# Kernel tuning notes

Measured on AMD Instinct MI355X. Metric: run time of the kernel, lower is better.

The kernel has to match this reference:

```python
import jax, jax.numpy as jnp
import numpy as np

HIDDEN = 1024
INTER = 4096
NUM_EXPERTS = 8
TOP_K = 2


def setup_inputs() -> dict:
    key = jax.random.key(0)
    ks = jax.random.split(key, 6)
    B, S = 4, 2048
    hidden_states = jax.random.normal(ks[0], (B, S, HIDDEN), dtype=jnp.float32)
    scale = 0.02
    # nn.Linear stores weight as [out, in]; y = x @ W.T + b
    gate_w = jax.random.normal(ks[1], (NUM_EXPERTS, HIDDEN), dtype=jnp.float32) * scale
    W1 = jax.random.normal(ks[2], (NUM_EXPERTS, INTER, HIDDEN), dtype=jnp.float32) * scale
    b1 = jax.random.normal(ks[3], (NUM_EXPERTS, INTER), dtype=jnp.float32) * scale
    W2 = jax.random.normal(ks[4], (NUM_EXPERTS, HIDDEN, INTER), dtype=jnp.float32) * scale
    b2 = jax.random.normal(ks[5], (NUM_EXPERTS, HIDDEN), dtype=jnp.float32) * scale
    return {"hidden_states": hidden_states, "gate_w": gate_w,
            "W1": W1, "b1": b1, "W2": W2, "b2": b2}


def reference(hidden_states, gate_w, W1, b1, W2, b2):
    B, S, H = hidden_states.shape
    x = hidden_states.reshape(-1, H)                      # [T, H]
    # Gating: top-k logits -> softmax over the k selected experts only
    gate_logits = x @ gate_w.T                            # [T, E]
    top_vals, top_idx = jax.lax.top_k(gate_logits, TOP_K) # [T, K]
    weights = jax.nn.softmax(top_vals, axis=-1)           # [T, K]
    # Per-token combine weight for each expert (0 if not selected)
    one_hot = jax.nn.one_hot(top_idx, NUM_EXPERTS, dtype=x.dtype)  # [T, K, E]
    combine = jnp.einsum("tk,tke->te", weights, one_hot)           # [T, E]
    # Expert MLPs: fixed small loop over experts (structurally distinct params)
    out = jnp.zeros_like(x)
    for e in range(NUM_EXPERTS):
        h = jax.nn.gelu(x @ W1[e].T + b1[e], approximate=False)  # [T, INTER]
        y = h @ W2[e].T + b2[e]                                   # [T, H]
        out = out + combine[:, e:e + 1] * y
    return out.reshape(B, S, H)
```

## Files before the change

### kernel.cpp

```cpp
#include <hip/hip_runtime.h>
#include <hip/hip_bf16.h>
#include <stdint.h>

#define HID 1024
#define INTER_ 4096
#define NE 8
#define NTOK 8192
#define NPAIR (NTOK * 2)
#define MAXT 72

using f32x4 = __attribute__((ext_vector_type(4))) float;
using bf16x8 = __attribute__((ext_vector_type(8))) __bf16;
using ushort8v = __attribute__((ext_vector_type(8))) unsigned short;

__device__ __forceinline__ unsigned short f2b(float f) {
  unsigned int u = __float_as_uint(f);
  u += 0x7fffu + ((u >> 16) & 1u);
  return (unsigned short)(u >> 16);
}
__device__ __forceinline__ float b2f(unsigned short u) {
  return __uint_as_float((unsigned int)u << 16);
}

__device__ __forceinline__ float gelu_f(float v) {
  float z = fabsf(v) * 0.70710678118654752f;
  float t = __builtin_amdgcn_rcpf(1.f + 0.3275911f * z);
  float p = t * (0.254829592f +
            t * (-0.284496736f +
            t * (1.421413741f +
            t * (-1.453152027f + t * 1.061405429f))));
  float er = 1.f - p * __expf(-z * z);
  er = copysignf(er, v);
  return 0.5f * v * (1.f + er);
}

#define GLD_LDS(gp, lp)                                                        \
  __builtin_amdgcn_global_load_lds(                                            \
      (const __attribute__((address_space(1))) unsigned int*)(const void*)(gp),\
      (__attribute__((address_space(3))) unsigned int*)(void*)(lp), 16, 0, 0)

#define WAITV(N) asm volatile("s_waitcnt vmcnt(" #N ")" ::: "memory")

__global__ __launch_bounds__(256) void gate_kernel(
    const float* __restrict__ x, const float* __restrict__ gw,
    int* __restrict__ topi, float* __restrict__ topw,
    unsigned short* __restrict__ xb)
{
  int gwave = (blockIdx.x * 256 + threadIdx.x) >> 6;
  int lane = threadIdx.x & 63;
  if (gwave >= NTOK) return;
  const float* xr = x + (size_t)gwave * HID;
  unsigned short* xo = xb + (size_t)gwave * HID;
  float acc[NE];
#pragma unroll
  for (int e = 0; e < NE; ++e) acc[e] = 0.f;
#pragma unroll
  for (int q = 0; q < 4; ++q) {
    float4 v = *reinterpret_cast<const float4*>(xr + q * 256 + lane * 4);
    ushort4 uv;
    uv.x = f2b(v.x); uv.y = f2b(v.y); uv.z = f2b(v.z); uv.w = f2b(v.w);
    *reinterpret_cast<ushort4*>(xo + q * 256 + lane * 4) = uv;
#pragma unroll
    for (int e = 0; e < NE; ++e) {
      float4 wv = *reinterpret_cast<const float4*>(gw + e * HID + q * 256 + lane * 4);
      acc[e] += v.x * wv.x + v.y * wv.y + v.z * wv.z + v.w * wv.w;
    }
  }
#pragma unroll
  for (int e = 0; e < NE; ++e) {
#pragma unroll
    for (int off = 32; off > 0; off >>= 1) acc[e] += __shfl_xor(acc[e], off);
  }
  if (lane == 0) {
    float v0 = -1e30f; int i0 = 0;
#pragma unroll
    for (int e = 0; e < NE; ++e) if (acc[e] > v0) { v0 = acc[e]; i0 = e; }
    float v1 = -1e30f; int i1 = 0;
#pragma unroll
    for (int e = 0; e < NE; ++e) if (e != i0 && acc[e] > v1) { v1 = acc[e]; i1 = e; }
    float e1 = __expf(v1 - v0);
    float s = 1.f + e1;
    topi[gwave * 2] = i0; topi[gwave * 2 + 1] = i1;
    topw[gwave * 2] = 1.f / s; topw[gwave * 2 + 1] = e1 / s;
  }
}

__global__ __launch_bounds__(256) void hist_kernel(const int* __restrict__ topi,
                                                   int* __restrict__ bcnt)
{
  int tid = threadIdx.x, blk = blockIdx.x;
  int t = blk * 256 + tid;
  int e0 = topi[t * 2], e1 = topi[t * 2 + 1];
  int w = tid >> 6, lane = tid & 63;
  __shared__ int wcnt[4][NE];
#pragma unroll
  for (int e = 0; e < NE; ++e) {
    unsigned long long m0 = __ballot(e0 == e);
    unsigned long long m1 = __ballot(e1 == e);
    if (lane == 0) wcnt[w][e] = __popcll(m0) + __popcll(m1);
  }
  __syncthreads();
  if (tid < NE) {
    int s = 0;
#pragma unroll
    for (int w2 = 0; w2 < 4; ++w2) s += wcnt[w2][tid];
    bcnt[blk * NE + tid] = s;
  }
}

__global__ void scan2_kernel(const int* __restrict__ bcnt, int* __restrict__ offs,
                             int* __restrict__ tile_e, int* __restrict__ tile_m,
                             int* __restrict__ ntile, int* __restrict__ gbase)
{
  __shared__ int cnts[NE];
  __shared__ int soffs[NE];
  int tid = threadIdx.x;
  if (tid < NE) {
    int s = 0;
#pragma unroll
    for (int b = 0; b < 32; ++b) s += bcnt[b * NE + tid];
    cnts[tid] = s;
  }
  __syncthreads();
  if (tid == 0) {
    int o = 0, tt = 0;
    for (int e = 0; e < NE; ++e) {
      offs[e] = o; soffs[e] = o;
      int c = cnts[e];
      for (int m = 0; m < c; m += 256) { tile_e[tt] = e; tile_m[tt] = m; ++tt; }
      o += c;
    }
    offs[NE] = o;
    *ntile = tt;
  }
  __syncthreads();
  if (tid < 32 * NE) {
    int b = tid >> 3, e = tid & 7;
    int g = soffs[e];
    for (int b2 = 0; b2 < b; ++b2) g += bcnt[b2 * NE + e];
    gbase[b * NE + e] = g;
  }
}

__global__ __launch_bounds__(256) void scatter2_kernel(
    const int* __restrict__ topi, const float* __restrict__ topw,
    const int* __restrict__ gbase,
    int* __restrict__ toklist, float* __restrict__ wlist, int* __restrict__ pos)
{
  int tid = threadIdx.x, blk = blockIdx.x;
  int t = blk * 256 + tid;
  int e0 = topi[t * 2], e1 = topi[t * 2 + 1];
  float w0 = topw[t * 2], w1 = topw[t * 2 + 1];
  int w = tid >> 6, lane = tid & 63;
  unsigned long long lt = (1ull << lane) - 1ull;
  unsigned long long le = lt | (1ull << lane);
  __shared__ int wcnt[4][NE];
  __shared__ int wbase[4][NE];
  int r0 = 0, r1 = 0;
#pragma unroll
  for (int e = 0; e < NE; ++e) {
    unsigned long long m0 = __ballot(e0 == e);
    unsigned long long m1 = __ballot(e1 == e);
    if (lane == 0) wcnt[w][e] = __popcll(m0) + __popcll(m1);
    if (e0 == e) r0 = __popcll(m0 & lt) + __popcll(m1 & lt);
    if (e1 == e) r1 = __popcll(m0 & le) + __popcll(m1 & lt);
  }
  __syncthreads();
  if (tid < 4 * NE) {
    int w2 = tid >> 3, e = tid & 7;
    int b = gbase[blk * NE + e];
    for (int w3 = 0; w3 < w2; ++w3) b += wcnt[w3][e];
    wbase[w2][e] = b;
  }
  __syncthreads();
  int P0 = wbase[w][e0] + r0;
  int P1 = wbase[w][e1] + r1;
  toklist[P0] = t; wlist[P0] = w0; pos[t * 2] = P0;
  toklist[P1] = t; wlist[P1] = w1; pos[t * 2 + 1] = P1;
}

__global__ __launch_bounds__(256) void cvtw_kernel(
    const float* __restrict__ W1, const float* __restrict__ W2,
    unsigned short* __restrict__ w1b, unsigned short* __restrict__ w2b, int n8)
{
  int half = gridDim.x >> 1;
  const float* src = (blockIdx.x < half) ? W1 : W2;
  unsigned short* dst = (blockIdx.x < half) ? w1b : w2b;
  int b0 = (blockIdx.x < half) ? blockIdx.x : blockIdx.x - half;
  int stride = half * 256;
  for (int i = b0 * 256 + threadIdx.x; i < n8; i += stride) {
    const float4* s = reinterpret_cast<const float4*>(src) + (size_t)i * 2;
    float4 a = s[0], b = s[1];
    ushort8v u;
    u[0] = f2b(a.x); u[1] = f2b(a.y); u[2] = f2b(a.z); u[3] = f2b(a.w);
    u[4] = f2b(b.x); u[5] = f2b(b.y); u[6] = f2b(b.z); u[7] = f2b(b.w);
    reinterpret_cast<ushort8v*>(dst)[i] = u;
  }
}


__global__ __launch_bounds__(512, 4) void gemm1_kernel(
    const unsigned short* __restrict__ xb, const unsigned short* __restrict__ w1b,
    const float* __restrict__ b1,
    const int* __restrict__ toklist, const int* __restrict__ offs,
    const int* __restrict__ tile_e, const int* __restrict__ tile_m,
    const int* __restrict__ ntile,
    unsigned short* __restrict__ hb)
{
  const int t = blockIdx.y;
  if (t >= *ntile) return;
  const int e = tile_e[t];
  const int m0 = tile_m[t];
  const int base = offs[e];
  const int cnt = offs[e + 1] - base;
  const int n0 = blockIdx.x * 128;

  __shared__ __align__(16) unsigned short As[3][256 * 32];
  __shared__ __align__(16) unsigned short Bs[3][128 * 32];

  const int tid = threadIdx.x;
  const int lane = tid & 63;
  const int w = tid >> 6;
  const int wr = w >> 1, wc = w & 1;

  const int r0 = tid >> 2;
  const int sl = tid & 3;
  const int scg = sl ^ ((r0 >> 1) & 3);
  const unsigned short* gA[2];
  const unsigned short* gB;
#pragma unroll
  for (int g = 0; g < 2; ++g) {
    int row = g * 128 + r0;
    int mrow = m0 + row; if (mrow >= cnt) mrow = cnt - 1;
    int tk = toklist[base + mrow];
    gA[g] = xb + (size_t)tk * HID + scg * 8;
  }
  gB = w1b + ((size_t)e * INTER_ + n0 + r0) * HID + scg * 8;

  int raq[4], rbq[4];
#pragma unroll
  for (int i = 0; i < 4; ++i) {
    int rA = wr * 64 + i * 16 + (lane & 15);
    raq[i] = rA * 32 + (((lane >> 4) ^ ((rA >> 1) & 3)) * 8);
    int rB = wc * 64 + i * 16 + (lane & 15);
    rbq[i] = rB * 32 + (((lane >> 4) ^ ((rB >> 1) & 3)) * 8);
  }

  f32x4 acc[4][4];
#pragma unroll
  for (int i = 0; i < 4; ++i)
#pragma unroll
    for (int j = 0; j < 4; ++j) acc[i][j] = (f32x4){0.f, 0.f, 0.f, 0.f};

  bf16x8 afr[4], bfr[4];

  auto stage = [&](int slot, int s) {
    const int kof = s * 32;
    GLD_LDS(gA[0] + kof, &As[slot][tid * 8]);
    GLD_LDS(gA[1] + kof, &As[slot][4096 + tid * 8]);
    GLD_LDS(gB + kof,    &Bs[slot][tid * 8]);
  };
  auto load_frags = [&](int slot) {
    const unsigned short* Ab = &As[slot][0];
    const unsigned short* Bb = &Bs[slot][0];
#pragma unroll
    for (int j = 0; j < 4; ++j) bfr[j] = *reinterpret_cast<const bf16x8*>(Bb + rbq[j]);
#pragma unroll
    for (int i = 0; i < 4; ++i) afr[i] = *reinterpret_cast<const bf16x8*>(Ab + raq[i]);
  };
  auto mfma_step = [&]() {
#pragma unroll
    for (int i = 0; i < 4; ++i)
#pragma unroll
      for (int j = 0; j < 4; ++j)
        acc[i][j] = __builtin_amdgcn_mfma_f32_16x16x32_bf16(afr[i], bfr[j], acc[i][j], 0, 0, 0);
  };

  const int NS = HID / 32;
  stage(0, 0); stage(1, 1);
  WAITV(3);
  __builtin_amdgcn_s_barrier();
  load_frags(0);
#pragma unroll 3
  for (int s = 0; s < NS - 2; ++s) {
    stage((s + 2) % 3, s + 2);
    WAITV(3);
    __builtin_amdgcn_s_barrier();
    mfma_step();
    load_frags((s + 1) % 3);
  }
  WAITV(0);
  __builtin_amdgcn_s_barrier();
  mfma_step();
  load_frags((NS - 1) % 3);
  mfma_step();

  float bias[4];
  const int colb = n0 + wc * 64 + (lane & 15);
#pragma unroll
  for (int j = 0; j < 4; ++j) bias[j] = b1[(size_t)e * INTER_ + colb + j * 16];
#pragma unroll
  for (int i = 0; i < 4; ++i) {
    int mbase = m0 + wr * 64 + i * 16 + (lane >> 4) * 4;
#pragma unroll
    for (int r = 0; r < 4; ++r) {
      int m = mbase + r;
      if (m < cnt) {
        unsigned short* hrow = hb + (size_t)(base + m) * INTER_ + colb;
#pragma unroll
        for (int j = 0; j < 4; ++j)
          hrow[j * 16] = f2b(gelu_f(acc[i][j][r] + bias[j]));
      }
    }
  }
}

__global__ __launch_bounds__(512, 4) void gemm2_kernel(
    const unsigned short* __restrict__ hb, const unsigned short* __restrict__ w2b,
    const int* __restrict__ offs,
    const int* __restrict__ tile_e, const int* __restrict__ tile_m,
    const int* __restrict__ ntile,
    unsigned short* __restrict__ part)
{
  const int h = blockIdx.x;
  const int xcd = h & 7;
  const int j = h >> 3;
  const int t = 9 * xcd + j % 9;
  const int nb = j / 9;
  if (t >= *ntile) return;
  const int e = tile_e[t];
  const int m0 = tile_m[t];
  const int base = offs[e];
  const int cnt = offs[e + 1] - base;
  const int n0 = nb * 128;
  const int kbase = blockIdx.z * (INTER_ / 2);

  __shared__ __align__(16) unsigned short As[3][256 * 32];
  __shared__ __align__(16) unsigned short Bs[3][128 * 32];

  const int tid = threadIdx.x;
  const int lane = tid & 63;
  const int w = tid >> 6;
  const int wr = w >> 1, wc = w & 1;

  const int r0 = tid >> 2;
  const int sl = tid & 3;
  const int scg = sl ^ ((r0 >> 1) & 3);
  const unsigned short* gA[2];
  const unsigned short* gB;
#pragma unroll
  for (int g = 0; g < 2; ++g) {
    int row = g * 128 + r0;
    int mrow = m0 + row; if (mrow >= cnt) mrow = cnt - 1;
    gA[g] = hb + (size_t)(base + mrow) * INTER_ + kbase + scg * 8;
  }
  gB = w2b + ((size_t)e * HID + n0 + r0) * INTER_ + kbase + scg * 8;

  int raq[4], rbq[4];
#pragma unroll
  for (int i = 0; i < 4; ++i) {
    int rA = wr * 64 + i * 16 + (lane & 15);
    raq[i] = rA * 32 + (((lane >> 4) ^ ((rA >> 1) & 3)) * 8);
    int rB = wc * 64 + i * 16 + (lane & 15);
    rbq[i] = rB * 32 + (((lane >> 4) ^ ((rB >> 1) & 3)) * 8);
  }

  f32x4 acc[4][4];
#pragma unroll
  for (int i = 0; i < 4; ++i)
#pragma unroll
    for (int j2 = 0; j2 < 4; ++j2) acc[i][j2] = (f32x4){0.f, 0.f, 0.f, 0.f};

  bf16x8 afr[4], bfr[4];

  auto stage = [&](int slot, int s) {
    const int kof = s * 32;
    GLD_LDS(gA[0] + kof, &As[slot][tid * 8]);
    GLD_LDS(gA[1] + kof, &As[slot][4096 + tid * 8]);
    GLD_LDS(gB + kof,    &Bs[slot][tid * 8]);
  };
  auto load_frags = [&](int slot) {
    const unsigned short* Ab = &As[slot][0];
    const unsigned short* Bb = &Bs[slot][0];
#pragma unroll
    for (int j2 = 0; j2 < 4; ++j2) bfr[j2] = *reinterpret_cast<const bf16x8*>(Bb + rbq[j2]);
#pragma unroll
    for (int i = 0; i < 4; ++i) afr[i] = *reinterpret_cast<const bf16x8*>(Ab + raq[i]);
  };
  auto mfma_step = [&]() {
#pragma unroll
    for (int i = 0; i < 4; ++i)
#pragma unroll
      for (int j2 = 0; j2 < 4; ++j2)
        acc[i][j2] = __builtin_amdgcn_mfma_f32_16x16x32_bf16(afr[i], bfr[j2], acc[i][j2], 0, 0, 0);
  };

  const int NS = (INTER_ / 2) / 32;
  stage(0, 0); stage(1, 1);
  WAITV(3);
  __builtin_amdgcn_s_barrier();
  load_frags(0);
#pragma unroll 3
  for (int s = 0; s < NS - 2; ++s) {
    stage((s + 2) % 3, s + 2);
    WAITV(3);
    __builtin_amdgcn_s_barrier();
    mfma_step();
    load_frags((s + 1) % 3);
  }
  WAITV(0);
  __builtin_amdgcn_s_barrier();
  mfma_step();
  load_frags((NS - 1) % 3);
  mfma_step();

  const int colb = n0 + wc * 64 + (lane & 15);
  unsigned short* pbase = part + (size_t)blockIdx.z * NPAIR * HID;
#pragma unroll
  for (int i = 0; i < 4; ++i) {
    int mbase = m0 + wr * 64 + i * 16 + (lane >> 4) * 4;
#pragma unroll
    for (int r = 0; r < 4; ++r) {
      int m = mbase + r;
      if (m < cnt) {
        unsigned short* prow = pbase + (size_t)(base + m) * HID + colb;
#pragma unroll
        for (int j2 = 0; j2 < 4; ++j2)
          prow[j2 * 16] = f2b(acc[i][j2][r]);
      }
    }
  }
}

__global__ __launch_bounds__(256) void combine_kernel(
    const unsigned short* __restrict__ part, const float* __restrict__ b2,
    const int* __restrict__ topi, const float* __restrict__ topw,
    const int* __restrict__ pos, float* __restrict__ out)
{
  int t = blockIdx.x * 4 + (threadIdx.x >> 6);
  int lane = threadIdx.x & 63;
  int c0 = lane * 16;
  float o[16];
#pragma unroll
  for (int c = 0; c < 16; ++c) o[c] = 0.f;
#pragma unroll
  for (int k = 0; k < 2; ++k) {
    int p = pos[t * 2 + k];
    int e = topi[t * 2 + k];
    float wk = topw[t * 2 + k];
    const unsigned short* rp0 = part + (size_t)p * HID + c0;
    const unsigned short* rp1 = part + ((size_t)NPAIR + p) * HID + c0;
    const float* bb = b2 + (size_t)e * HID + c0;
#pragma unroll
    for (int v = 0; v < 2; ++v) {
      ushort8v a = *reinterpret_cast<const ushort8v*>(rp0 + v * 8);
      ushort8v b = *reinterpret_cast<const ushort8v*>(rp1 + v * 8);
      float4 bb0 = *reinterpret_cast<const float4*>(bb + v * 8);
      float4 bb1 = *reinterpret_cast<const float4*>(bb + v * 8 + 4);
      o[v * 8 + 0] += wk * (b2f(a[0]) + b2f(b[0]) + bb0.x);
      o[v * 8 + 1] += wk * (b2f(a[1]) + b2f(b[1]) + bb0.y);
      o[v * 8 + 2] += wk * (b2f(a[2]) + b2f(b[2]) + bb0.z);
      o[v * 8 + 3] += wk * (b2f(a[3]) + b2f(b[3]) + bb0.w);
      o[v * 8 + 4] += wk * (b2f(a[4]) + b2f(b[4]) + bb1.x);
      o[v * 8 + 5] += wk * (b2f(a[5]) + b2f(b[5]) + bb1.y);
      o[v * 8 + 6] += wk * (b2f(a[6]) + b2f(b[6]) + bb1.z);
      o[v * 8 + 7] += wk * (b2f(a[7]) + b2f(b[7]) + bb1.w);
    }
  }
  float4* op = reinterpret_cast<float4*>(out + (size_t)t * HID + c0);
#pragma unroll
  for (int v = 0; v < 4; ++v)
    op[v] = make_float4(o[v * 4], o[v * 4 + 1], o[v * 4 + 2], o[v * 4 + 3]);
}

extern "C" void kernel_launch(void* const* d_in, const int* in_sizes, int n_in,
                              void* d_out, int out_size, void* d_ws, size_t ws_size,
                              hipStream_t stream) {
  const float* x  = (const float*)d_in[0];
  const float* gw = (const float*)d_in[1];
  const float* W1 = (const float*)d_in[2];
  const float* b1 = (const float*)d_in[3];
  const float* W2 = (const float*)d_in[4];
  const float* b2 = (const float*)d_in[5];
  float* out = (float*)d_out;

  char* ws = (char*)d_ws;
  size_t off = 0;
  auto alloc = [&](size_t bytes) -> void* {
    void* p = ws + off;
    off += (bytes + 255) & ~(size_t)255;
    return p;
  };
  unsigned short* hb   = (unsigned short*)alloc((size_t)NPAIR * INTER_ * 2);
  unsigned short* xb   = (unsigned short*)alloc((size_t)NTOK * HID * 2);
  unsigned short* w1b  = (unsigned short*)alloc((size_t)NE * INTER_ * HID * 2);
  unsigned short* w2b  = (unsigned short*)alloc((size_t)NE * HID * INTER_ * 2);
  unsigned short* part = (unsigned short*)alloc((size_t)2 * NPAIR * HID * 2);
  int*   toklist = (int*)alloc(NPAIR * 4);
  float* wlist   = (float*)alloc(NPAIR * 4);
  int*   topi    = (int*)alloc(NTOK * 2 * 4);
  float* topw    = (float*)alloc(NTOK * 2 * 4);
  int*   pos     = (int*)alloc(NTOK * 2 * 4);
  int*   bcnt    = (int*)alloc(32 * NE * 4);
  int*   gbase   = (int*)alloc(32 * NE * 4);
  int*   offs    = (int*)alloc(64);
  int*   tile_e  = (int*)alloc(MAXT * 4);
  int*   tile_m  = (int*)alloc(MAXT * 4);
  int*   ntile   = (int*)alloc(64);

  gate_kernel<<<NTOK / 4, 256, 0, stream>>>(x, gw, topi, topw, xb);
  hist_kernel<<<32, 256, 0, stream>>>(topi, bcnt);
  scan2_kernel<<<1, 256, 0, stream>>>(bcnt, offs, tile_e, tile_m, ntile, gbase);
  scatter2_kernel<<<32, 256, 0, stream>>>(topi, topw, gbase, toklist, wlist, pos);
  cvtw_kernel<<<4096, 256, 0, stream>>>(W1, W2, w1b, w2b, NE * INTER_ * HID / 8);
  gemm1_kernel<<<dim3(INTER_ / 128, MAXT), 512, 0, stream>>>(
      xb, w1b, b1, toklist, offs, tile_e, tile_m, ntile, hb);
  gemm2_kernel<<<dim3(8 * MAXT, 1, 2), 512, 0, stream>>>(
      hb, w2b, offs, tile_e, tile_m, ntile, part);
  combine_kernel<<<NTOK / 4, 256, 0, stream>>>(part, b2, topi, topw, pos, out);
}
```

Before: 490.1 us.

## Retile gemm1 to 128x256 tiles with 256-thread blocks and separate tile list

Gemm1 now uses 128-row token tiles by 256-column output tiles with 4 waves per block, where it previously used 256x128 tiles with 8 waves. A second, finer tile list (128-row granularity) is built in the scan kernel for it. Each wave computes a 64x128 subtile, and B fragments are loaded per column inside the MFMA loop, with the MFMA step moved ahead of the next stage issue. The aim is less padding waste for uneven expert counts and more MFMA work per LDS read, at the cost of more accumulator registers and lower occupancy.

```diff
diff --git a/kernel.cpp b/kernel.cpp
--- a/kernel.cpp
+++ b/kernel.cpp
@@ -8,6 +8,7 @@
 #define NTOK 8192
 #define NPAIR (NTOK * 2)
 #define MAXT 72
+#define MAXT1 136
 
 using f32x4 = __attribute__((ext_vector_type(4))) float;
 using bf16x8 = __attribute__((ext_vector_type(8))) __bf16;
@@ -110,7 +111,9 @@
 
 __global__ void scan2_kernel(const int* __restrict__ bcnt, int* __restrict__ offs,
                              int* __restrict__ tile_e, int* __restrict__ tile_m,
-                             int* __restrict__ ntile, int* __restrict__ gbase)
+                             int* __restrict__ ntile,
+                             int* __restrict__ tile1_e, int* __restrict__ tile1_m,
+                             int* __restrict__ ntile1, int* __restrict__ gbase)
 {
   __shared__ int cnts[NE];
   __shared__ int soffs[NE];
@@ -123,15 +126,17 @@
   }
   __syncthreads();
   if (tid == 0) {
-    int o = 0, tt = 0;
+    int o = 0, tt = 0, t1 = 0;
     for (int e = 0; e < NE; ++e) {
       offs[e] = o; soffs[e] = o;
       int c = cnts[e];
       for (int m = 0; m < c; m += 256) { tile_e[tt] = e; tile_m[tt] = m; ++tt; }
+      for (int m = 0; m < c; m += 128) { tile1_e[t1] = e; tile1_m[t1] = m; ++t1; }
       o += c;
     }
     offs[NE] = o;
     *ntile = tt;
+    *ntile1 = t1;
   }
   __syncthreads();
   if (tid < 32 * NE) {
@@ -198,25 +203,24 @@
   }
 }
 
-
-__global__ __launch_bounds__(512, 4) void gemm1_kernel(
+__global__ __launch_bounds__(256, 2) void gemm1_kernel(
     const unsigned short* __restrict__ xb, const unsigned short* __restrict__ w1b,
     const float* __restrict__ b1,
     const int* __restrict__ toklist, const int* __restrict__ offs,
-    const int* __restrict__ tile_e, const int* __restrict__ tile_m,
-    const int* __restrict__ ntile,
+    const int* __restrict__ tile1_e, const int* __restrict__ tile1_m,
+    const int* __restrict__ ntile1,
     unsigned short* __restrict__ hb)
 {
   const int t = blockIdx.y;
-  if (t >= *ntile) return;
-  const int e = tile_e[t];
-  const int m0 = tile_m[t];
+  if (t >= *ntile1) return;
+  const int e = tile1_e[t];
+  const int m0 = tile1_m[t];
   const int base = offs[e];
   const int cnt = offs[e + 1] - base;
-  const int n0 = blockIdx.x * 128;
-
-  __shared__ __align__(16) unsigned short As[3][256 * 32];
-  __shared__ __align__(16) unsigned short Bs[3][128 * 32];
+  const int n0 = blockIdx.x * 256;
+
+  __shared__ __align__(16) unsigned short As[3][128 * 32];
+  __shared__ __align__(16) unsigned short Bs[3][256 * 32];
 
   const int tid = threadIdx.x;
   const int lane = tid & 63;
@@ -227,78 +231,85 @@
   const int sl = tid & 3;
   const int scg = sl ^ ((r0 >> 1) & 3);
   const unsigned short* gA[2];
-  const unsigned short* gB;
+  const unsigned short* gB[4];
 #pragma unroll
   for (int g = 0; g < 2; ++g) {
-    int row = g * 128 + r0;
+    int row = g * 64 + r0;
     int mrow = m0 + row; if (mrow >= cnt) mrow = cnt - 1;
     int tk = toklist[base + mrow];
     gA[g] = xb + (size_t)tk * HID + scg * 8;
   }
-  gB = w1b + ((size_t)e * INTER_ + n0 + r0) * HID + scg * 8;
-
-  int raq[4], rbq[4];
+#pragma unroll
+  for (int q = 0; q < 4; ++q)
+    gB[q] = w1b + ((size_t)e * INTER_ + n0 + q * 64 + r0) * HID + scg * 8;
+
+  int raq[4], rbq[8];
 #pragma unroll
   for (int i = 0; i < 4; ++i) {
     int rA = wr * 64 + i * 16 + (lane & 15);
     raq[i] = rA * 32 + (((lane >> 4) ^ ((rA >> 1) & 3)) * 8);
-    int rB = wc * 64 + i * 16 + (lane & 15);
-    rbq[i] = rB * 32 + (((lane >> 4) ^ ((rB >> 1) & 3)) * 8);
-  }
-
-  f32x4 acc[4][4];
+  }
+#pragma unroll
+  for (int j = 0; j < 8; ++j) {
+    int rB = wc * 128 + j * 16 + (lane & 15);
+    rbq[j] = rB * 32 + (((lane >> 4) ^ ((rB >> 1) & 3)) * 8);
+  }
+
+  f32x4 acc[4][8];
 #pragma unroll
   for (int i = 0; i < 4; ++i)
 #pragma unroll
-    for (int j = 0; j < 4; ++j) acc[i][j] = (f32x4){0.f, 0.f, 0.f, 0.f};
-
-  bf16x8 afr[4], bfr[4];
+    for (int j = 0; j < 8; ++j) acc[i][j] = (f32x4){0.f, 0.f, 0.f, 0.f};
+
+  bf16x8 afr[4];
 
   auto stage = [&](int slot, int s) {
     const int kof = s * 32;
     GLD_LDS(gA[0] + kof, &As[slot][tid * 8]);
-    GLD_LDS(gA[1] + kof, &As[slot][4096 + tid * 8]);
-    GLD_LDS(gB + kof,    &Bs[slot][tid * 8]);
-  };
-  auto load_frags = [&](int slot) {
-    const unsigned short* Ab = &As[slot][0];
+    GLD_LDS(gA[1] + kof, &As[slot][2048 + tid * 8]);
+#pragma unroll
+    for (int q = 0; q < 4; ++q)
+      GLD_LDS(gB[q] + kof, &Bs[slot][q * 2048 + tid * 8]);
+  };
+  auto load_afr = [&](int slot) {
+#pragma unroll
+    for (int i = 0; i < 4; ++i)
+      afr[i] = *reinterpret_cast<const bf16x8*>(&As[slot][raq[i]]);
+  };
+  auto mfma_step = [&](int slot) {
     const unsigned short* Bb = &Bs[slot][0];
 #pragma unroll
-    for (int j = 0; j < 4; ++j) bfr[j] = *reinterpret_cast<const bf16x8*>(Bb + rbq[j]);
-#pragma unroll
-    for (int i = 0; i < 4; ++i) afr[i] = *reinterpret_cast<const bf16x8*>(Ab + raq[i]);
-  };
-  auto mfma_step = [&]() {
-#pragma unroll
-    for (int i = 0; i < 4; ++i)
-#pragma unroll
-      for (int j = 0; j < 4; ++j)
-        acc[i][j] = __builtin_amdgcn_mfma_f32_16x16x32_bf16(afr[i], bfr[j], acc[i][j], 0, 0, 0);
+    for (int j = 0; j < 8; ++j) {
+      bf16x8 bfr = *reinterpret_cast<const bf16x8*>(Bb + rbq[j]);
+#pragma unroll
+      for (int i = 0; i < 4; ++i)
+        acc[i][j] = __builtin_amdgcn_mfma_f32_16x16x32_bf16(afr[i], bfr, acc[i][j], 0, 0, 0);
+    }
   };
 
   const int NS = HID / 32;
   stage(0, 0); stage(1, 1);
-  WAITV(3);
+  WAITV(6);
   __builtin_amdgcn_s_barrier();
-  load_frags(0);
+  load_afr(0);
 #pragma unroll 3
   for (int s = 0; s < NS - 2; ++s) {
+    mfma_step(s % 3);
     stage((s + 2) % 3, s + 2);
-    WAITV(3);
+    WAITV(6);
     __builtin_amdgcn_s_barrier();
-    mfma_step();
-    load_frags((s + 1) % 3);
-  }
+    load_afr((s + 1) % 3);
+  }
+  mfma_step((NS - 2) % 3);
   WAITV(0);
   __builtin_amdgcn_s_barrier();
-  mfma_step();
-  load_frags((NS - 1) % 3);
-  mfma_step();
-
-  float bias[4];
-  const int colb = n0 + wc * 64 + (lane & 15);
-#pragma unroll
-  for (int j = 0; j < 4; ++j) bias[j] = b1[(size_t)e * INTER_ + colb + j * 16];
+  load_afr((NS - 1) % 3);
+  mfma_step((NS - 1) % 3);
+
+  float bias[8];
+  const int colb = n0 + wc * 128 + (lane & 15);
+#pragma unroll
+  for (int j = 0; j < 8; ++j) bias[j] = b1[(size_t)e * INTER_ + colb + j * 16];
 #pragma unroll
   for (int i = 0; i < 4; ++i) {
     int mbase = m0 + wr * 64 + i * 16 + (lane >> 4) * 4;
@@ -308,7 +319,7 @@
       if (m < cnt) {
         unsigned short* hrow = hb + (size_t)(base + m) * INTER_ + colb;
 #pragma unroll
-        for (int j = 0; j < 4; ++j)
+        for (int j = 0; j < 8; ++j)
           hrow[j * 16] = f2b(gelu_f(acc[i][j][r] + bias[j]));
       }
     }
@@ -507,14 +518,18 @@
   int*   tile_e  = (int*)alloc(MAXT * 4);
   int*   tile_m  = (int*)alloc(MAXT * 4);
   int*   ntile   = (int*)alloc(64);
+  int*   tile1_e = (int*)alloc(MAXT1 * 4);
+  int*   tile1_m = (int*)alloc(MAXT1 * 4);
+  int*   ntile1  = (int*)alloc(64);
 
   gate_kernel<<<NTOK / 4, 256, 0, stream>>>(x, gw, topi, topw, xb);
   hist_kernel<<<32, 256, 0, stream>>>(topi, bcnt);
-  scan2_kernel<<<1, 256, 0, stream>>>(bcnt, offs, tile_e, tile_m, ntile, gbase);
+  scan2_kernel<<<1, 256, 0, stream>>>(bcnt, offs, tile_e, tile_m, ntile,
+                                      tile1_e, tile1_m, ntile1, gbase);
   scatter2_kernel<<<32, 256, 0, stream>>>(topi, topw, gbase, toklist, wlist, pos);
   cvtw_kernel<<<4096, 256, 0, stream>>>(W1, W2, w1b, w2b, NE * INTER_ * HID / 8);
-  gemm1_kernel<<<dim3(INTER_ / 128, MAXT), 512, 0, stream>>>(
-      xb, w1b, b1, toklist, offs, tile_e, tile_m, ntile, hb);
+  gemm1_kernel<<<dim3(INTER_ / 256, MAXT1), 256, 0, stream>>>(
+      xb, w1b, b1, toklist, offs, tile1_e, tile1_m, ntile1, hb);
   gemm2_kernel<<<dim3(8 * MAXT, 1, 2), 512, 0, stream>>>(
       hb, w2b, offs, tile_e, tile_m, ntile, part);
   combine_kernel<<<NTOK / 4, 256, 0, stream>>>(part, b2, topi, topw, pos, out);
```

After: 496.1 us. No clear change (+1.2%).
